# Kernel tuning notes

Hardware: AMD Instinct MI355X
Metric: run time of the kernel (lower is better)

The kernel has to match this reference:

```python
import jax, jax.numpy as jnp
import numpy as np

B, D_IN, T = 8, 1024, 2048
K, D_CB = 8192, 8
COMMIT = 0.005
CB_LOSS_W = 1.0
EPS = 1e-12  # F.normalize eps


def _wn(v, g):
    # torch weight_norm(dim=0) on a 1x1 Conv1d: w = g * v / ||v|| per output row
    return g[:, None] * v / jnp.linalg.norm(v, axis=1, keepdims=True)


def _l2n(x):
    return x / jnp.maximum(jnp.linalg.norm(x, axis=-1, keepdims=True), EPS)


def setup_inputs() -> dict:
    key = jax.random.key(0)
    ks = jax.random.split(key, 8)
    return {
        "z": jax.random.normal(ks[0], (B, D_IN, T), dtype=jnp.float32),
        "in_v": jax.random.normal(ks[1], (D_CB, D_IN), dtype=jnp.float32) * 0.02,
        "in_g": jnp.ones((D_CB,), dtype=jnp.float32),
        "in_b": jnp.zeros((D_CB,), dtype=jnp.float32),
        "out_v": jax.random.normal(ks[2], (D_IN, D_CB), dtype=jnp.float32) * 0.02,
        "out_g": jnp.ones((D_IN,), dtype=jnp.float32),
        "out_b": jnp.zeros((D_IN,), dtype=jnp.float32),
        "codebook": jax.random.normal(ks[3], (K, D_CB), dtype=jnp.float32),
    }


def reference(z, in_v, in_g, in_b, out_v, out_g, out_b, codebook):
    sg = jax.lax.stop_gradient
    # in_project: weight-normed 1x1 conv == matmul over channel dim
    w_in = _wn(in_v, in_g)
    z_e = jnp.einsum('oi,bit->bot', w_in, z) + in_b[None, :, None]  # [B, D_CB, T]

    # decode_latents
    enc = jnp.transpose(z_e, (0, 2, 1)).reshape(-1, D_CB)  # (B*T, D_CB)
    enc_n = _l2n(enc)
    cb_n = _l2n(codebook)
    dist = (jnp.sum(enc_n**2, axis=1, keepdims=True)
            - 2.0 * enc_n @ cb_n.T
            + jnp.sum(cb_n**2, axis=1)[None, :])  # (B*T, K)
    indices = jnp.argmin(dist, axis=1).reshape(B, T)  # [B, T]
    z_q = jnp.transpose(codebook[indices], (0, 2, 1))  # [B, D_CB, T] (unnormalized codebook)

    # training losses (per-batch means over (d, t))
    commit_loss = jnp.mean((z_e - sg(z_q)) ** 2, axis=(1, 2)) * COMMIT
    codebook_loss = jnp.mean((z_q - sg(z_e)) ** 2, axis=(1, 2)) * CB_LOSS_W

    # straight-through estimator
    z_q_st = z_e + sg(z_q - z_e)

    # out_project
    w_out = _wn(out_v, out_g)
    z_q_out = jnp.einsum('od,bdt->bot', w_out, z_q_st) + out_b[None, :, None]  # [B, D_IN, T]
    return (z_q_out, commit_loss, codebook_loss, indices, z_e)
```

## Files before the change

kernel.cpp:

```cpp
#include <hip/hip_runtime.h>
#include <math.h>
#include <stdint.h>

#define BB    8
#define DIN   1024
#define TT    2048
#define KK    8192
#define DCB   8
#define NPOS  (BB*TT)
#define KCHUNKS 64
#define KCH     (KK/KCHUNKS)
#define MARGIN  6e-4f

#define OFF_ZQOUT  0
#define OFF_COMMIT 16777216
#define OFF_CBLOSS 16777224
#define OFF_IDX    16777232
#define OFF_ZE     16793616

typedef short s8v __attribute__((ext_vector_type(8)));
typedef float f4v __attribute__((ext_vector_type(4)));

__device__ __forceinline__ unsigned short f2bf(float f) {
    unsigned u = __float_as_uint(f);
    u += 0x7FFF + ((u >> 16) & 1);
    return (unsigned short)(u >> 16);
}
__device__ __forceinline__ float bf2f(unsigned short h) {
    return __uint_as_float(((unsigned)h) << 16);
}

__global__ __launch_bounds__(256) void k_prep(
    const float* __restrict__ in_v, const float* __restrict__ in_g,
    const float* __restrict__ out_v, const float* __restrict__ out_g,
    const float* __restrict__ cb,
    double* __restrict__ w_in_d, float* __restrict__ w_out_f,
    double* __restrict__ cb_n, double* __restrict__ s_k,
    unsigned short* __restrict__ cb16, float* __restrict__ skp_f)
{
    __shared__ double red[256];
    int tid = threadIdx.x;
    int blk = blockIdx.x;

    if (blk < 8) {
        int r = blk;
        double s = 0.0;
        for (int i = tid; i < DIN; i += 256) {
            double v = (double)in_v[r*DIN + i];
            s += v*v;
        }
        red[tid] = s; __syncthreads();
        for (int off = 128; off > 0; off >>= 1) {
            if (tid < off) red[tid] += red[tid+off];
            __syncthreads();
        }
        double scale = (double)in_g[r] / sqrt(red[0]);
        for (int i = tid; i < DIN; i += 256)
            w_in_d[r*DIN + i] = scale * (double)in_v[r*DIN + i];
    } else if (blk < 12) {
        int o = (blk-8)*256 + tid;
        float vv[DCB];
        double s = 0.0;
        #pragma unroll
        for (int d = 0; d < DCB; ++d) {
            vv[d] = out_v[o*DCB + d];
            s += (double)vv[d]*(double)vv[d];
        }
        double scale = (double)out_g[o] / sqrt(s);
        #pragma unroll
        for (int d = 0; d < DCB; ++d)
            w_out_f[o*DCB + d] = (float)(scale * (double)vv[d]);
    } else {
        int k = (blk-12)*256 + tid;
        double v[DCB]; double s = 0.0;
        #pragma unroll
        for (int d = 0; d < DCB; ++d) {
            v[d] = (double)cb[k*DCB + d];
            s += v[d]*v[d];
        }
        double nrm = sqrt(s);
        if (nrm < 1e-12) nrm = 1e-12;
        double s2 = 0.0;
        #pragma unroll
        for (int d = 0; d < DCB; ++d) {
            double t = v[d] / nrm;
            cb_n[(size_t)k*DCB + d] = t;
            s2 += t*t;
            float cf = (float)t;
            unsigned short bh = f2bf(cf);
            unsigned short bl = f2bf(cf - bf2f(bh));
            cb16[(size_t)k*16 + d]     = bh;
            cb16[(size_t)k*16 + 8 + d] = bl;
        }
        s_k[k] = s2;
        skp_f[k] = (float)(s2 + 4.0);
    }
}

__global__ __launch_bounds__(256) void k_inproj(
    const float* __restrict__ z, const double* __restrict__ w_in_d,
    const float* __restrict__ in_b,
    float* __restrict__ ze_out, double* __restrict__ enc_n,
    double* __restrict__ q_s, unsigned short* __restrict__ enc16)
{
    __shared__ double wl[DIN*DCB];
    __shared__ double red[2048];

    int tid = threadIdx.x;
    for (int x = tid; x < DIN*DCB; x += 256) wl[x] = w_in_d[x];
    __syncthreads();

    int p = tid & 31;
    int q = tid >> 5;
    int pos = blockIdx.x*32 + p;
    int b = pos >> 11, t = pos & (TT-1);

    const float* zp = z + ((size_t)b*DIN + (size_t)q*128)*TT + t;
    double acc[DCB] = {0,0,0,0,0,0,0,0};
    for (int ii = 0; ii < 128; ++ii) {
        double zv = (double)zp[(size_t)ii*TT];
        int wbase = q*128 + ii;
        #pragma unroll
        for (int o = 0; o < DCB; ++o) acc[o] += wl[o*DIN + wbase] * zv;
    }
    #pragma unroll
    for (int o = 0; o < DCB; ++o) red[(q*32 + p)*DCB + o] = acc[o];
    __syncthreads();

    int p2 = tid >> 3, o2 = tid & 7;
    double s = 0.0;
    for (int q2 = 0; q2 < 8; ++q2) s += red[(q2*32 + p2)*DCB + o2];
    s += (double)in_b[o2];
    __syncthreads();
    red[p2*DCB + o2] = s;
    __syncthreads();

    if (tid < 32) {
        int pos3 = blockIdx.x*32 + tid;
        int b3 = pos3 >> 11, t3 = pos3 & (TT-1);
        double v[DCB]; double n2 = 0.0;
        #pragma unroll
        for (int o = 0; o < DCB; ++o) {
            v[o] = red[tid*DCB + o];
            n2 += v[o]*v[o];
            ze_out[((size_t)b3*DCB + o)*TT + t3] = (float)v[o];
        }
        double nrm = sqrt(n2);
        if (nrm < 1e-12) nrm = 1e-12;
        double s2 = 0.0;
        #pragma unroll
        for (int o = 0; o < DCB; ++o) {
            double e = v[o] / nrm;
            enc_n[(size_t)pos3*DCB + o] = e;
            s2 += e*e;
            float ef = (float)(-2.0 * e);
            unsigned short ah = f2bf(ef);
            unsigned short al = f2bf(ef - bf2f(ah));
            enc16[(size_t)pos3*16 + o]     = ah;
            enc16[(size_t)pos3*16 + 8 + o] = al;
        }
        q_s[pos3] = s2;
    }
}

#define SCR_QB 64
#define SCR_CB 8
__global__ __launch_bounds__(256) void k_screen(
    const unsigned short* __restrict__ enc16,
    const unsigned short* __restrict__ cb16,
    const float* __restrict__ skp_f,
    int* __restrict__ d1key)
{
    __shared__ unsigned short cbl[SCR_CB*KCH*16];
    __shared__ float skl[SCR_CB*KCH];
    int tid = threadIdx.x;
    int cg = blockIdx.y;

    {
        const uint4* src = (const uint4*)(cb16 + (size_t)cg*SCR_CB*KCH*16);
        uint4* dst = (uint4*)cbl;
        for (int x = tid; x < SCR_CB*KCH*2; x += 256) dst[x] = src[x];
        const float* ss = skp_f + cg*SCR_CB*KCH;
        for (int x = tid; x < SCR_CB*KCH; x += 256) skl[x] = ss[x];
    }
    __syncthreads();

    int lane = tid & 63;
    int wv   = tid >> 6;
    int col  = lane & 15, quad = lane >> 4;
    int qbase = blockIdx.x*SCR_QB + wv*16;

    s8v a;
    {
        const s8v* ap = (const s8v*)(enc16 + ((size_t)(qbase + col))*16 + (quad==1 ? 8 : 0));
        a = *ap;
        if (quad == 3) { s8v zz = {0,0,0,0,0,0,0,0}; a = zz; }
    }
    int bsel = (quad == 2) ? 1 : 0;

    for (int c2 = 0; c2 < SCR_CB; ++c2) {
        int d0 = 0x7F800000, d1r = 0x7F800000, d2r = 0x7F800000, d3r = 0x7F800000;
        const s8v* bp = (const s8v*)(cbl + c2*KCH*16);
        const float* sp = skl + c2*KCH;
        #pragma unroll
        for (int t = 0; t < 8; ++t) {
            int n = t*16 + col;
            s8v bfr = bp[n*2 + bsel];
            float sk = sp[n];
            f4v acc = {sk, sk, sk, sk};
            acc = __builtin_amdgcn_mfma_f32_16x16x32_bf16(a, bfr, acc, 0, 0, 0);
            d0  = min(d0,  (int)((__float_as_uint(acc.x) & 0xFFFFFF80u) | (unsigned)n));
            d1r = min(d1r, (int)((__float_as_uint(acc.y) & 0xFFFFFF80u) | (unsigned)n));
            d2r = min(d2r, (int)((__float_as_uint(acc.z) & 0xFFFFFF80u) | (unsigned)n));
            d3r = min(d3r, (int)((__float_as_uint(acc.w) & 0xFFFFFF80u) | (unsigned)n));
        }
        #pragma unroll
        for (int off = 1; off < 16; off <<= 1) {
            d0  = min(d0,  __shfl_xor(d0,  off, 64));
            d1r = min(d1r, __shfl_xor(d1r, off, 64));
            d2r = min(d2r, __shfl_xor(d2r, off, 64));
            d3r = min(d3r, __shfl_xor(d3r, off, 64));
        }
        if (col == 0) {
            int chunk = cg*SCR_CB + c2;
            int qrow  = qbase + quad*4;
            int* dst = d1key + (size_t)qrow*KCHUNKS + chunk;
            dst[0*KCHUNKS] = d0;
            dst[1*KCHUNKS] = d1r;
            dst[2*KCHUNKS] = d2r;
            dst[3*KCHUNKS] = d3r;
        }
    }
}

__global__ __launch_bounds__(256) void k_verify(
    const int* __restrict__ d1key,
    const double* __restrict__ enc_n, const double* __restrict__ q_s,
    const double* __restrict__ cb_n, const double* __restrict__ s_k,
    const float* __restrict__ cb, const float* __restrict__ ze,
    float* __restrict__ idx_f, int* __restrict__ idx_i,
    double* __restrict__ loss_q)
{
    int tid = threadIdx.x;
    int lane = tid & 63;
    int pos = blockIdx.x*4 + (tid >> 6);

    int myk = d1key[(size_t)pos*KCHUNKS + lane];
    int m = myk;
    #pragma unroll
    for (int off = 1; off < 64; off <<= 1) m = min(m, __shfl_xor(m, off, 64));
    float thr = __int_as_float(m & 0xFFFFFF80) + MARGIN;
    bool scan = __int_as_float(myk & 0xFFFFFF80) <= thr;
    unsigned long long mask = __ballot(scan);

    double e[DCB];
    #pragma unroll
    for (int d = 0; d < DCB; ++d) e[d] = enc_n[(size_t)pos*DCB + d];
    double qs = q_s[pos];

    double bd = 1e300; int bi = 0x7FFFFFFF;
    while (mask) {
        int c = __ffsll((long long)mask) - 1;
        mask &= mask - 1;
        #pragma unroll
        for (int r = 0; r < KCH/64; ++r) {
            int k = c*KCH + r*64 + lane;
            const double* cp = cb_n + (size_t)k*DCB;
            double dot = e[0]*cp[0] + e[1]*cp[1] + e[2]*cp[2] + e[3]*cp[3]
                       + e[4]*cp[4] + e[5]*cp[5] + e[6]*cp[6] + e[7]*cp[7];
            double dist = qs - 2.0*dot + s_k[k];
            if (dist < bd || (dist == bd && k < bi)) { bd = dist; bi = k; }
        }
    }
    #pragma unroll
    for (int off = 1; off < 64; off <<= 1) {
        double od = __shfl_xor(bd, off, 64);
        int    oi = __shfl_xor(bi, off, 64);
        if (od < bd || (od == bd && oi < bi)) { bd = od; bi = oi; }
    }
    if (lane == 0) {
        int b = pos >> 11, t = pos & (TT-1);
        idx_f[pos] = (float)bi;
        idx_i[pos] = bi;
        double ssum = 0.0;
        #pragma unroll
        for (int d = 0; d < DCB; ++d) {
            double zev = (double)ze[((size_t)b*DCB + d)*TT + t];
            double zqv = (double)cb[bi*DCB + d];
            double diff = zev - zqv;
            ssum += diff*diff;
        }
        loss_q[pos] = ssum;
    }
}

__global__ __launch_bounds__(256) void k_losses(
    const double* __restrict__ loss_q,
    float* __restrict__ commit_out, float* __restrict__ cbloss_out)
{
    __shared__ double red[256];
    int tid = threadIdx.x;
    int b = blockIdx.x;
    double s = 0.0;
    for (int i = tid; i < TT; i += 256) s += loss_q[(size_t)b*TT + i];
    red[tid] = s; __syncthreads();
    for (int off = 128; off > 0; off >>= 1) {
        if (tid < off) red[tid] += red[tid+off];
        __syncthreads();
    }
    if (tid == 0) {
        double m = red[0] / (double)(DCB*TT);
        commit_out[b] = (float)(m * 0.005);
        cbloss_out[b] = (float)m;
    }
}

__global__ __launch_bounds__(256) void k_out_proj(
    const float* __restrict__ cb, const float* __restrict__ ze,
    const int* __restrict__ idx_i, const float* __restrict__ w_out,
    const float* __restrict__ out_b, float* __restrict__ zq_out)
{
    __shared__ float wl[128*DCB];
    __shared__ float bl[128];
    int tid = threadIdx.x;

    int oc = blockIdx.y;
    int obase = oc*128;
    for (int x = tid; x < 128*DCB; x += 256) wl[x] = w_out[obase*DCB + x];
    for (int x = tid; x < 128; x += 256) bl[x] = out_b[obase + x];
    __syncthreads();

    int pos = blockIdx.x*256 + tid;
    int b = pos >> 11, t = pos & (TT-1);
    int ki = idx_i[pos];
    float zq[DCB];
    #pragma unroll
    for (int d = 0; d < DCB; ++d) {
        float zev = ze[((size_t)b*DCB + d)*TT + t];
        float zqv = cb[ki*DCB + d];
        zq[d] = zev + (zqv - zev);
    }
    float* outp = zq_out + ((size_t)b*DIN + obase)*TT + t;
    for (int oo = 0; oo < 128; ++oo) {
        float acc = 0.f;
        #pragma unroll
        for (int d = 0; d < DCB; ++d) acc += wl[oo*DCB + d]*zq[d];
        acc += bl[oo];
        outp[(size_t)oo*TT] = acc;
    }
}

extern "C" void kernel_launch(void* const* d_in, const int* in_sizes, int n_in,
                              void* d_out, int out_size, void* d_ws, size_t ws_size,
                              hipStream_t stream)
{
    const float* z        = (const float*)d_in[0];
    const float* in_v     = (const float*)d_in[1];
    const float* in_g     = (const float*)d_in[2];
    const float* in_b     = (const float*)d_in[3];
    const float* out_v    = (const float*)d_in[4];
    const float* out_g    = (const float*)d_in[5];
    const float* out_b    = (const float*)d_in[6];
    const float* codebook = (const float*)d_in[7];

    float* out = (float*)d_out;
    float* zq_out_p  = out + OFF_ZQOUT;
    float* commit_p  = out + OFF_COMMIT;
    float* cbloss_p  = out + OFF_CBLOSS;
    float* idx_p     = out + OFF_IDX;
    float* ze_p      = out + OFF_ZE;

    double* w_in_d = (double*)d_ws;
    double* cb_n   = w_in_d + DCB*DIN;
    double* s_k    = cb_n + (size_t)KK*DCB;
    double* enc_n  = s_k + KK;
    double* q_s    = enc_n + (size_t)NPOS*DCB;
    double* loss_q = q_s + NPOS;
    float*  w_out  = (float*)(loss_q + NPOS);
    float*  skp_f  = w_out + DCB*DIN;
    unsigned short* cb16  = (unsigned short*)(skp_f + KK);
    unsigned short* enc16 = cb16 + (size_t)KK*16;
    int*    d1key  = (int*)(enc16 + (size_t)NPOS*16);
    int*    idx_i  = d1key + (size_t)NPOS*KCHUNKS;

    k_prep<<<44, 256, 0, stream>>>(in_v, in_g, out_v, out_g, codebook,
                                   w_in_d, w_out, cb_n, s_k, cb16, skp_f);
    k_inproj<<<NPOS/32, 256, 0, stream>>>(z, w_in_d, in_b, ze_p, enc_n, q_s, enc16);
    k_screen<<<dim3(NPOS/SCR_QB, KCHUNKS/SCR_CB), 256, 0, stream>>>(
        enc16, cb16, skp_f, d1key);
    k_verify<<<NPOS/4, 256, 0, stream>>>(d1key, enc_n, q_s, cb_n, s_k,
                                         codebook, ze_p, idx_p, idx_i, loss_q);
    k_losses<<<BB, 256, 0, stream>>>(loss_q, commit_p, cbloss_p);
    k_out_proj<<<dim3(NPOS/256, DIN/128), 256, 0, stream>>>(
        codebook, ze_p, idx_i, w_out, out_b, zq_out_p);
}
```

Before: 204.4 us.

## Rewrite input projection in fp32 with vectorized loads and shuffle reductions

Result: faster. 185.8 us (-9.1%).

```diff
diff --git a/kernel.cpp b/kernel.cpp
--- a/kernel.cpp
+++ b/kernel.cpp
@@ -34,7 +34,7 @@
     const float* __restrict__ in_v, const float* __restrict__ in_g,
     const float* __restrict__ out_v, const float* __restrict__ out_g,
     const float* __restrict__ cb,
-    double* __restrict__ w_in_d, float* __restrict__ w_out_f,
+    float* __restrict__ w_in_f, float* __restrict__ w_out_f,
     double* __restrict__ cb_n, double* __restrict__ s_k,
     unsigned short* __restrict__ cb16, float* __restrict__ skp_f)
 {
@@ -56,7 +56,7 @@
         }
         double scale = (double)in_g[r] / sqrt(red[0]);
         for (int i = tid; i < DIN; i += 256)
-            w_in_d[r*DIN + i] = scale * (double)in_v[r*DIN + i];
+            w_in_f[i*DCB + r] = (float)(scale * (double)in_v[r*DIN + i]);
     } else if (blk < 12) {
         int o = (blk-8)*256 + tid;
         float vv[DCB];
@@ -98,69 +98,105 @@
 }
 
 __global__ __launch_bounds__(256) void k_inproj(
-    const float* __restrict__ z, const double* __restrict__ w_in_d,
+    const float* __restrict__ z, const float* __restrict__ w_in_f,
     const float* __restrict__ in_b,
     float* __restrict__ ze_out, double* __restrict__ enc_n,
     double* __restrict__ q_s, unsigned short* __restrict__ enc16)
 {
-    __shared__ double wl[DIN*DCB];
-    __shared__ double red[2048];
-
-    int tid = threadIdx.x;
-    for (int x = tid; x < DIN*DCB; x += 256) wl[x] = w_in_d[x];
+    __shared__ float sm[DIN*DCB];
+
+    int tid = threadIdx.x;
+    {
+        const uint4* src = (const uint4*)w_in_f;
+        uint4* dst = (uint4*)sm;
+        #pragma unroll
+        for (int x = 0; x < 8; ++x) dst[tid + 256*x] = src[tid + 256*x];
+    }
     __syncthreads();
 
-    int p = tid & 31;
-    int q = tid >> 5;
-    int pos = blockIdx.x*32 + p;
-    int b = pos >> 11, t = pos & (TT-1);
-
-    const float* zp = z + ((size_t)b*DIN + (size_t)q*128)*TT + t;
-    double acc[DCB] = {0,0,0,0,0,0,0,0};
-    for (int ii = 0; ii < 128; ++ii) {
-        double zv = (double)zp[(size_t)ii*TT];
-        int wbase = q*128 + ii;
-        #pragma unroll
-        for (int o = 0; o < DCB; ++o) acc[o] += wl[o*DIN + wbase] * zv;
-    }
-    #pragma unroll
-    for (int o = 0; o < DCB; ++o) red[(q*32 + p)*DCB + o] = acc[o];
+    int p = tid & 7;
+    int q = tid >> 3;
+    int pos0 = blockIdx.x*32;
+    int b = pos0 >> 11, t0 = pos0 & (TT-1);
+
+    const float* zp = z + ((size_t)b*DIN + q)*TT + t0 + p*4;
+
+    float acc[DCB][4];
+    #pragma unroll
+    for (int o = 0; o < DCB; ++o)
+        #pragma unroll
+        for (int j = 0; j < 4; ++j) acc[o][j] = 0.f;
+
+    #pragma unroll
+    for (int ii = 0; ii < 32; ++ii) {
+        f4v zv = *(const f4v*)(zp + (size_t)ii*32*TT);
+        const f4v* wp = (const f4v*)(sm + (ii*32 + q)*DCB);
+        f4v w0 = wp[0], w1 = wp[1];
+        #pragma unroll
+        for (int j = 0; j < 4; ++j) {
+            acc[0][j] += w0[0]*zv[j];
+            acc[1][j] += w0[1]*zv[j];
+            acc[2][j] += w0[2]*zv[j];
+            acc[3][j] += w0[3]*zv[j];
+            acc[4][j] += w1[0]*zv[j];
+            acc[5][j] += w1[1]*zv[j];
+            acc[6][j] += w1[2]*zv[j];
+            acc[7][j] += w1[3]*zv[j];
+        }
+    }
+
+    #pragma unroll
+    for (int o = 0; o < DCB; ++o)
+        #pragma unroll
+        for (int j = 0; j < 4; ++j) {
+            float v = acc[o][j];
+            v += __shfl_xor(v, 8, 64);
+            v += __shfl_xor(v, 16, 64);
+            v += __shfl_xor(v, 32, 64);
+            acc[o][j] = v;
+        }
+
     __syncthreads();
-
-    int p2 = tid >> 3, o2 = tid & 7;
+    int lane = tid & 63, wv = tid >> 6;
+    if ((lane >> 3) == 0) {
+        float* rp = sm + wv*256 + p*32;
+        #pragma unroll
+        for (int o = 0; o < DCB; ++o)
+            #pragma unroll
+            for (int j = 0; j < 4; ++j) rp[o*4 + j] = acc[o][j];
+    }
+    __syncthreads();
+
+    int o2 = tid & 7, p32 = tid >> 3;
     double s = 0.0;
-    for (int q2 = 0; q2 < 8; ++q2) s += red[(q2*32 + p2)*DCB + o2];
+    #pragma unroll
+    for (int w2 = 0; w2 < 4; ++w2)
+        s += (double)sm[w2*256 + (p32 >> 2)*32 + o2*4 + (p32 & 3)];
     s += (double)in_b[o2];
-    __syncthreads();
-    red[p2*DCB + o2] = s;
-    __syncthreads();
-
-    if (tid < 32) {
-        int pos3 = blockIdx.x*32 + tid;
-        int b3 = pos3 >> 11, t3 = pos3 & (TT-1);
-        double v[DCB]; double n2 = 0.0;
-        #pragma unroll
-        for (int o = 0; o < DCB; ++o) {
-            v[o] = red[tid*DCB + o];
-            n2 += v[o]*v[o];
-            ze_out[((size_t)b3*DCB + o)*TT + t3] = (float)v[o];
-        }
-        double nrm = sqrt(n2);
-        if (nrm < 1e-12) nrm = 1e-12;
-        double s2 = 0.0;
-        #pragma unroll
-        for (int o = 0; o < DCB; ++o) {
-            double e = v[o] / nrm;
-            enc_n[(size_t)pos3*DCB + o] = e;
-            s2 += e*e;
-            float ef = (float)(-2.0 * e);
-            unsigned short ah = f2bf(ef);
-            unsigned short al = f2bf(ef - bf2f(ah));
-            enc16[(size_t)pos3*16 + o]     = ah;
-            enc16[(size_t)pos3*16 + 8 + o] = al;
-        }
-        q_s[pos3] = s2;
-    }
+
+    int pos = pos0 + p32;
+    int b3 = pos >> 11, t3 = pos & (TT-1);
+    ze_out[((size_t)b3*DCB + o2)*TT + t3] = (float)s;
+
+    double n2 = s*s;
+    n2 += __shfl_xor(n2, 1, 64);
+    n2 += __shfl_xor(n2, 2, 64);
+    n2 += __shfl_xor(n2, 4, 64);
+    double nrm = sqrt(n2);
+    if (nrm < 1e-12) nrm = 1e-12;
+    double e = s / nrm;
+    enc_n[(size_t)pos*DCB + o2] = e;
+    double s2 = e*e;
+    s2 += __shfl_xor(s2, 1, 64);
+    s2 += __shfl_xor(s2, 2, 64);
+    s2 += __shfl_xor(s2, 4, 64);
+    if (o2 == 0) q_s[pos] = s2;
+
+    float ef = (float)(-2.0 * e);
+    unsigned short ah = f2bf(ef);
+    unsigned short al = f2bf(ef - bf2f(ah));
+    enc16[(size_t)pos*16 + o2]     = ah;
+    enc16[(size_t)pos*16 + 8 + o2] = al;
 }
 
 #define SCR_QB 64
@@ -370,8 +406,8 @@
     float* idx_p     = out + OFF_IDX;
     float* ze_p      = out + OFF_ZE;
 
-    double* w_in_d = (double*)d_ws;
-    double* cb_n   = w_in_d + DCB*DIN;
+    float*  w_in_f = (float*)d_ws;
+    double* cb_n   = (double*)d_ws + DCB*DIN;
     double* s_k    = cb_n + (size_t)KK*DCB;
     double* enc_n  = s_k + KK;
     double* q_s    = enc_n + (size_t)NPOS*DCB;
@@ -384,8 +420,8 @@
     int*    idx_i  = d1key + (size_t)NPOS*KCHUNKS;
 
     k_prep<<<44, 256, 0, stream>>>(in_v, in_g, out_v, out_g, codebook,
-                                   w_in_d, w_out, cb_n, s_k, cb16, skp_f);
-    k_inproj<<<NPOS/32, 256, 0, stream>>>(z, w_in_d, in_b, ze_p, enc_n, q_s, enc16);
+                                   w_in_f, w_out, cb_n, s_k, cb16, skp_f);
+    k_inproj<<<NPOS/32, 256, 0, stream>>>(z, w_in_f, in_b, ze_p, enc_n, q_s, enc16);
     k_screen<<<dim3(NPOS/SCR_QB, KCHUNKS/SCR_CB), 256, 0, stream>>>(
         enc16, cb16, skp_f, d1key);
     k_verify<<<NPOS/4, 256, 0, stream>>>(d1key, enc_n, q_s, cb_n, s_k,
```
